# Kernel optimization log

Hardware: AMD Instinct MI355X
Metric: run time of the kernel (lower is better)

The kernel has to match this reference:

```python
import jax, jax.numpy as jnp
import numpy as np

B, S, D = 2, 2048, 1024
H, DK = 16, 64          # heads, d_k (= d_v)
DH = 4096               # FFN hidden
EPS = 1e-5


def _layer_norm(x, gamma, beta):
    mu = jnp.mean(x, axis=-1, keepdims=True)
    var = jnp.var(x, axis=-1, keepdims=True)
    return (x - mu) * jax.lax.rsqrt(var + EPS) * gamma + beta


def setup_inputs() -> dict:
    key = jax.random.key(0)
    ks = jax.random.split(key, 8)
    s = lambda fan_in: 1.0 / np.sqrt(fan_in)
    return {
        "x": jax.random.normal(ks[0], (B, S, D), dtype=jnp.float32),
        # NOTE: source module uses W_q for queries, keys AND values (bug kept faithfully),
        # so W_k / W_v are never used and are not materialized.
        "Wq": jax.random.normal(ks[1], (D, H * DK), dtype=jnp.float32) * s(D),
        "bq": jnp.zeros((H * DK,), dtype=jnp.float32),
        "Wo": jax.random.normal(ks[2], (H * DK, D), dtype=jnp.float32) * s(H * DK),
        "bo": jnp.zeros((D,), dtype=jnp.float32),
        "ln1_g": jnp.ones((D,), dtype=jnp.float32),
        "ln1_b": jnp.zeros((D,), dtype=jnp.float32),
        "W1": jax.random.normal(ks[3], (D, DH), dtype=jnp.float32) * s(D),
        "b1": jnp.zeros((DH,), dtype=jnp.float32),
        "W2": jax.random.normal(ks[4], (DH, D), dtype=jnp.float32) * s(DH),
        "b2": jnp.zeros((D,), dtype=jnp.float32),
        "ln2_g": jnp.ones((D,), dtype=jnp.float32),
        "ln2_b": jnp.zeros((D,), dtype=jnp.float32),
    }


def reference(x, Wq, bq, Wo, bo, ln1_g, ln1_b, W1, b1, W2, b2, ln2_g, ln2_b):
    residual = x
    # projections: q, k, v all use W_q (faithful to source)
    q = (x @ Wq + bq).reshape(B, S, H, DK)
    k = (x @ Wq + bq).reshape(B, S, H, DK)
    v = (x @ Wq + bq).reshape(B, S, H, DK)
    # scores scaled by sqrt(sequence_length), as in the source
    scale = 1.0 / jnp.sqrt(jnp.float32(S))
    scores = jnp.einsum("bqhd,bkhd->bhqk", q, k) * scale
    probs = jax.nn.softmax(scores, axis=-1)
    attn = jnp.einsum("bhqk,bkhd->bqhd", probs, v).reshape(B, S, H * DK)
    attn = attn @ Wo + bo
    # dropout is identity in eval mode
    x = _layer_norm(attn + residual, ln1_g, ln1_b)
    residual = x
    h = jax.nn.relu(x @ W1 + b1)
    x = h @ W2 + b2
    x = _layer_norm(x + residual, ln2_g, ln2_b)
    return x
```

## Files before the change

kernel.cpp:

```cpp
#include <hip/hip_runtime.h>
#include <stdint.h>


typedef unsigned short u16;
typedef __attribute__((ext_vector_type(8))) short v8s;
typedef __attribute__((ext_vector_type(4))) float v4f;

#define AS1 __attribute__((address_space(1)))
#define AS3 __attribute__((address_space(3)))

__device__ __forceinline__ void gl_lds16(const u16* g, u16* l) {
  __builtin_amdgcn_global_load_lds((const AS1 void*)g, (AS3 void*)l, 16, 0, 0);
}

__device__ __forceinline__ float bf2f(u16 u) {
  union { uint32_t i; float f; } v; v.i = ((uint32_t)u) << 16; return v.f;
}
__device__ __forceinline__ u16 f2bf(float f) {
  union { float f; uint32_t i; } v; v.f = f;
  uint32_t x = v.i;
  return (u16)((x + 0x7FFFu + ((x >> 16) & 1u)) >> 16);
}
__device__ __forceinline__ uint32_t fbits(float f) {
  union { float f; uint32_t u; } v; v.f = f; return v.u;
}

__global__ __launch_bounds__(256) void cvt_f2b(
    const float* __restrict__ src, u16* __restrict__ dst, int n4) {
  int i = (blockIdx.x * 256 + threadIdx.x);
  if (i < n4) {
    float4 v = *(const float4*)(src + (size_t)i * 4);
    ushort4 o;
    o.x = f2bf(v.x); o.y = f2bf(v.y); o.z = f2bf(v.z); o.w = f2bf(v.w);
    *(ushort4*)(dst + (size_t)i * 4) = o;
  }
}

__global__ __launch_bounds__(256) void transpose_f2b(
    const float* __restrict__ src, u16* __restrict__ dst,
    int R, int C, int ld_s, int ld_d) {
  __shared__ float tile[32][33];
  const int tx = threadIdx.x & 31, ty = threadIdx.x >> 5;
  const int c0 = blockIdx.x * 32, r0 = blockIdx.y * 32;
#pragma unroll
  for (int j = 0; j < 32; j += 8)
    tile[ty + j][tx] = src[(size_t)(r0 + ty + j) * ld_s + c0 + tx];
  __syncthreads();
#pragma unroll
  for (int j = 0; j < 32; j += 8)
    dst[(size_t)(c0 + ty + j) * ld_d + r0 + tx] = f2bf(tile[tx][ty + j]);
}

__global__ __launch_bounds__(256) void transpose_b2b(
    const u16* __restrict__ src, u16* __restrict__ dst,
    int R, int C, int ld_s, int ld_d) {
  __shared__ u16 tile[32][33];
  const int tx = threadIdx.x & 31, ty = threadIdx.x >> 5;
  const int c0 = blockIdx.x * 32, r0 = blockIdx.y * 32;
#pragma unroll
  for (int j = 0; j < 32; j += 8)
    tile[ty + j][tx] = src[(size_t)(r0 + ty + j) * ld_s + c0 + tx];
  __syncthreads();
#pragma unroll
  for (int j = 0; j < 32; j += 8)
    dst[(size_t)(c0 + ty + j) * ld_d + r0 + tx] = tile[tx][ty + j];
}

__global__ __launch_bounds__(256) void gemm_g1(
    const u16* __restrict__ A, const u16* __restrict__ Bt,
    const float* __restrict__ bias, void* __restrict__ C,
    int M, int N, int K, int relu, int accum, int out_f32) {
  __shared__ u16 As[2][4096];
  __shared__ u16 Bs[2][4096];
  const int tid = threadIdx.x;
  const int w = tid >> 6, l = tid & 63;
  const int lane16 = l & 15, kgrp = l >> 4;
  const int m0 = blockIdx.y * 128, n0 = blockIdx.x * 128;
  const int wr = (w >> 1) * 64, wc = (w & 1) * 64;

  const int sr = w * 32 + (l >> 2);
  const int sc = l & 3;
  const int sgc = sc ^ ((sr & 3) ^ ((sr >> 2) & 3));
  const u16* gA = A + (size_t)(m0 + sr) * K + 8 * sgc;
  const u16* gB = Bt + (size_t)(n0 + sr) * K + 8 * sgc;
  const size_t rstep = (size_t)16 * K;
  const int fl = (lane16 & 3) ^ ((lane16 >> 2) & 3);

  v4f acc[4][4];
#pragma unroll
  for (int i = 0; i < 4; i++)
#pragma unroll
    for (int j = 0; j < 4; j++)
#pragma unroll
      for (int r = 0; r < 4; r++) acc[i][j][r] = 0.f;

  gl_lds16(gA, &As[0][w * 1024]);
  gl_lds16(gA + rstep, &As[0][w * 1024 + 512]);
  gl_lds16(gB, &Bs[0][w * 1024]);
  gl_lds16(gB + rstep, &Bs[0][w * 1024 + 512]);

  int cur = 0;
  for (int k0 = 0; k0 < K; k0 += 32) {
    __syncthreads();
    if (k0 + 32 < K) {
      int nxt = cur ^ 1;
      gl_lds16(gA + k0 + 32, &As[nxt][w * 1024]);
      gl_lds16(gA + k0 + 32 + rstep, &As[nxt][w * 1024 + 512]);
      gl_lds16(gB + k0 + 32, &Bs[nxt][w * 1024]);
      gl_lds16(gB + k0 + 32 + rstep, &Bs[nxt][w * 1024 + 512]);
    }
    v8s a[4], b[4];
#pragma unroll
    for (int mi = 0; mi < 4; mi++)
      a[mi] = *(const v8s*)(&As[cur][(wr + mi * 16 + lane16) * 32 + 8 * (kgrp ^ fl)]);
#pragma unroll
    for (int ni = 0; ni < 4; ni++)
      b[ni] = *(const v8s*)(&Bs[cur][(wc + ni * 16 + lane16) * 32 + 8 * (kgrp ^ fl)]);
#pragma unroll
    for (int mi = 0; mi < 4; mi++)
#pragma unroll
      for (int ni = 0; ni < 4; ni++)
        acc[mi][ni] = __builtin_amdgcn_mfma_f32_16x16x32_bf16(a[mi], b[ni], acc[mi][ni], 0, 0, 0);
    cur ^= 1;
  }

#pragma unroll
  for (int ni = 0; ni < 4; ni++) {
    int col = n0 + wc + ni * 16 + lane16;
    float bv = bias ? bias[col] : 0.f;
#pragma unroll
    for (int mi = 0; mi < 4; mi++) {
      int row = m0 + wr + mi * 16 + kgrp * 4;
#pragma unroll
      for (int r = 0; r < 4; r++) {
        float v = acc[mi][ni][r] + bv;
        if (relu) v = fmaxf(v, 0.f);
        size_t idx = (size_t)(row + r) * N + col;
        if (out_f32) {
          float* Cf = (float*)C;
          if (accum) v += Cf[idx];
          Cf[idx] = v;
        } else {
          ((u16*)C)[idx] = f2bf(v);
        }
      }
    }
  }
}

__global__ __launch_bounds__(256) void gemm_g2(
    const u16* __restrict__ A, const u16* __restrict__ Bt,
    const float* __restrict__ bias, void* __restrict__ C,
    int M, int N, int K, int relu, int accum, int out_f32) {
  __shared__ u16 As[2][4096];
  __shared__ u16 Bs[2][2048];
  const int tid = threadIdx.x;
  const int w = tid >> 6, l = tid & 63;
  const int lane16 = l & 15, kgrp = l >> 4;
  const int m0 = blockIdx.y * 128, n0 = blockIdx.x * 64;
  const int wr = (w >> 1) * 64, wc = (w & 1) * 32;

  const int srA = w * 32 + (l >> 2);
  const int srB = w * 16 + (l >> 2);
  const int sc = l & 3;
  const int gcA = sc ^ ((srA & 3) ^ ((srA >> 2) & 3));
  const int gcB = sc ^ ((srB & 3) ^ ((srB >> 2) & 3));
  const u16* gA = A + (size_t)(m0 + srA) * K + 8 * gcA;
  const u16* gB = Bt + (size_t)(n0 + srB) * K + 8 * gcB;
  const size_t rstep = (size_t)16 * K;
  const int fl = (lane16 & 3) ^ ((lane16 >> 2) & 3);

  v4f acc[4][2];
#pragma unroll
  for (int i = 0; i < 4; i++)
#pragma unroll
    for (int j = 0; j < 2; j++)
#pragma unroll
      for (int r = 0; r < 4; r++) acc[i][j][r] = 0.f;

  gl_lds16(gA, &As[0][w * 1024]);
  gl_lds16(gA + rstep, &As[0][w * 1024 + 512]);
  gl_lds16(gB, &Bs[0][w * 512]);

  int cur = 0;
  for (int k0 = 0; k0 < K; k0 += 32) {
    __syncthreads();
    if (k0 + 32 < K) {
      int nxt = cur ^ 1;
      gl_lds16(gA + k0 + 32, &As[nxt][w * 1024]);
      gl_lds16(gA + k0 + 32 + rstep, &As[nxt][w * 1024 + 512]);
      gl_lds16(gB + k0 + 32, &Bs[nxt][w * 512]);
    }
    v8s a[4], b[2];
#pragma unroll
    for (int mi = 0; mi < 4; mi++)
      a[mi] = *(const v8s*)(&As[cur][(wr + mi * 16 + lane16) * 32 + 8 * (kgrp ^ fl)]);
#pragma unroll
    for (int ni = 0; ni < 2; ni++)
      b[ni] = *(const v8s*)(&Bs[cur][(wc + ni * 16 + lane16) * 32 + 8 * (kgrp ^ fl)]);
#pragma unroll
    for (int mi = 0; mi < 4; mi++)
#pragma unroll
      for (int ni = 0; ni < 2; ni++)
        acc[mi][ni] = __builtin_amdgcn_mfma_f32_16x16x32_bf16(a[mi], b[ni], acc[mi][ni], 0, 0, 0);
    cur ^= 1;
  }

#pragma unroll
  for (int ni = 0; ni < 2; ni++) {
    int col = n0 + wc + ni * 16 + lane16;
    float bv = bias ? bias[col] : 0.f;
#pragma unroll
    for (int mi = 0; mi < 4; mi++) {
      int row = m0 + wr + mi * 16 + kgrp * 4;
#pragma unroll
      for (int r = 0; r < 4; r++) {
        float v = acc[mi][ni][r] + bv;
        if (relu) v = fmaxf(v, 0.f);
        size_t idx = (size_t)(row + r) * N + col;
        if (out_f32) {
          float* Cf = (float*)C;
          if (accum) v += Cf[idx];
          Cf[idx] = v;
        } else {
          ((u16*)C)[idx] = f2bf(v);
        }
      }
    }
  }
}

__global__ __launch_bounds__(256) void attn_kernel(
    const u16* __restrict__ Q,
    const u16* __restrict__ Qt,
    u16* __restrict__ O) {
  __shared__ u16 KV[2][8192];
  __shared__ __align__(16) u16 Ps[4][2304];
  const int tid = threadIdx.x;
  const int w = tid >> 6, l = tid & 63;
  const int l16 = l & 15, kgrp = l >> 4;
  const int bh = blockIdx.y, b = bh >> 4, h = bh & 15;
  const int q0 = blockIdx.x * 128;
  const size_t rowQ = (size_t)(b * 2048 + q0 + w * 32);
  const float cexp = 1.4426950408889634f / 45.254833995939045f;

  const int srow = w * 8 + (l >> 3);
  const int sch8 = 8 * ((l & 7) ^ (srow & 7));
  const u16* gK0 = Q + (size_t)(b * 2048 + srow) * 1024 + h * 64 + sch8;
  const u16* gK1 = gK0 + (size_t)32 * 1024;
  const u16* gV0 = Qt + (size_t)(h * 64 + srow) * 4096 + b * 2048 + sch8;
  const u16* gV1 = gV0 + (size_t)32 * 4096;

  v8s qb[2][2];
#pragma unroll
  for (int nj = 0; nj < 2; nj++)
#pragma unroll
    for (int ks = 0; ks < 2; ks++) {
      v8s t = *(const v8s*)(Q + (rowQ + nj * 16 + l16) * 1024 + h * 64 + ks * 32 + kgrp * 8);
#pragma unroll
      for (int j = 0; j < 8; j++) t[j] = (short)f2bf(bf2f((u16)t[j]) * cexp);
      qb[nj][ks] = t;
    }

  v4f o[2][4];
  float ls[2] = {0.f, 0.f};
#pragma unroll
  for (int i = 0; i < 2; i++)
#pragma unroll
    for (int j = 0; j < 4; j++)
#pragma unroll
      for (int r = 0; r < 4; r++) o[i][j][r] = 0.f;

  gl_lds16(gK0, &KV[0][w * 512]);
  gl_lds16(gK1, &KV[0][2048 + w * 512]);
  gl_lds16(gV0, &KV[0][4096 + w * 512]);
  gl_lds16(gV1, &KV[0][4096 + 2048 + w * 512]);

  u16* Pw = &Ps[w][0];
  int cur = 0;
  for (int kb = 0; kb < 2048; kb += 64) {
    __syncthreads();
    if (kb + 64 < 2048) {
      int nxt = cur ^ 1;
      gl_lds16(gK0 + (size_t)(kb + 64) * 1024, &KV[nxt][w * 512]);
      gl_lds16(gK1 + (size_t)(kb + 64) * 1024, &KV[nxt][2048 + w * 512]);
      gl_lds16(gV0 + (kb + 64), &KV[nxt][4096 + w * 512]);
      gl_lds16(gV1 + (kb + 64), &KV[nxt][4096 + 2048 + w * 512]);
    }
    const u16* Ks = &KV[cur][0];
    const u16* Vt = &KV[cur][4096];

    v4f st[4][2];
#pragma unroll
    for (int i = 0; i < 4; i++)
#pragma unroll
      for (int j = 0; j < 2; j++)
#pragma unroll
        for (int r = 0; r < 4; r++) st[i][j][r] = 0.f;
#pragma unroll
    for (int ks = 0; ks < 2; ks++) {
      v8s ka[4];
#pragma unroll
      for (int mi = 0; mi < 4; mi++)
        ka[mi] = *(const v8s*)(Ks + (mi * 16 + l16) * 64 + 8 * ((ks * 4 + kgrp) ^ (l16 & 7)));
#pragma unroll
      for (int mi = 0; mi < 4; mi++)
#pragma unroll
        for (int nj = 0; nj < 2; nj++)
          st[mi][nj] = __builtin_amdgcn_mfma_f32_16x16x32_bf16(ka[mi], qb[nj][ks], st[mi][nj], 0, 0, 0);
    }

#pragma unroll
    for (int mi = 0; mi < 4; mi++)
#pragma unroll
      for (int nj = 0; nj < 2; nj++) {
        float p0 = __builtin_amdgcn_exp2f(st[mi][nj][0]);
        float p1 = __builtin_amdgcn_exp2f(st[mi][nj][1]);
        float p2 = __builtin_amdgcn_exp2f(st[mi][nj][2]);
        float p3 = __builtin_amdgcn_exp2f(st[mi][nj][3]);
        ls[nj] += (p0 + p1) + (p2 + p3);
        uint2 pk;
        pk.x = __builtin_amdgcn_perm(fbits(p1), fbits(p0), 0x07060302u);
        pk.y = __builtin_amdgcn_perm(fbits(p3), fbits(p2), 0x07060302u);
        *(uint2*)(Pw + (nj * 16 + l16) * 72 + mi * 16 + kgrp * 4) = pk;
      }

#pragma unroll
    for (int t = 0; t < 2; t++) {
      v8s pa[2], vb[4];
#pragma unroll
      for (int nj = 0; nj < 2; nj++)
        pa[nj] = *(const v8s*)(Pw + (nj * 16 + l16) * 72 + t * 32 + kgrp * 8);
#pragma unroll
      for (int ni = 0; ni < 4; ni++)
        vb[ni] = *(const v8s*)(Vt + (ni * 16 + l16) * 64 + 8 * ((t * 4 + kgrp) ^ (l16 & 7)));
#pragma unroll
      for (int nj = 0; nj < 2; nj++)
#pragma unroll
        for (int ni = 0; ni < 4; ni++)
          o[nj][ni] = __builtin_amdgcn_mfma_f32_16x16x32_bf16(pa[nj], vb[ni], o[nj][ni], 0, 0, 0);
    }
    cur ^= 1;
  }

#pragma unroll
  for (int nj = 0; nj < 2; nj++) {
    float t = ls[nj];
    t += __shfl_xor(t, 16, 64);
    t += __shfl_xor(t, 32, 64);
    ls[nj] = t;
  }

#pragma unroll
  for (int nj = 0; nj < 2; nj++) {
#pragma unroll
    for (int r = 0; r < 4; r++) {
      float den = __shfl(ls[nj], kgrp * 4 + r, 64);
      float rden = 1.f / den;
#pragma unroll
      for (int ni = 0; ni < 4; ni++) {
        O[(rowQ + nj * 16 + kgrp * 4 + r) * 1024 + h * 64 + ni * 16 + l16] =
            f2bf(o[nj][ni][r] * rden);
      }
    }
  }
}

__global__ __launch_bounds__(256) void ln_residual(
    const void* __restrict__ Y, const void* __restrict__ Xr,
    const float* __restrict__ g, const float* __restrict__ bb,
    void* __restrict__ out, int yf, int xf, int of) {
  const int row = blockIdx.x, tid = threadIdx.x;
  const size_t base = (size_t)row * 1024;
  float v[4], s = 0.f, sq = 0.f;
#pragma unroll
  for (int i = 0; i < 4; i++) {
    int c = tid + i * 256;
    float ya = yf ? ((const float*)Y)[base + c] : bf2f(((const u16*)Y)[base + c]);
    float xa = xf ? ((const float*)Xr)[base + c] : bf2f(((const u16*)Xr)[base + c]);
    float x = ya + xa;
    v[i] = x; s += x; sq += x * x;
  }
#pragma unroll
  for (int off = 32; off >= 1; off >>= 1) {
    s += __shfl_down(s, off, 64);
    sq += __shfl_down(sq, off, 64);
  }
  __shared__ float rs[4], rq[4];
  const int w = tid >> 6, l = tid & 63;
  if (l == 0) { rs[w] = s; rq[w] = sq; }
  __syncthreads();
  s = rs[0] + rs[1] + rs[2] + rs[3];
  sq = rq[0] + rq[1] + rq[2] + rq[3];
  const float mu = s * (1.f / 1024.f);
  const float var = sq * (1.f / 1024.f) - mu * mu;
  const float rstd = rsqrtf(var + 1e-5f);
#pragma unroll
  for (int i = 0; i < 4; i++) {
    int c = tid + i * 256;
    float r = (v[i] - mu) * rstd * g[c] + bb[c];
    if (of) ((float*)out)[base + c] = r;
    else ((u16*)out)[base + c] = f2bf(r);
  }
}

extern "C" void kernel_launch(void* const* d_in, const int* in_sizes, int n_in,
                              void* d_out, int out_size, void* d_ws, size_t ws_size,
                              hipStream_t stream) {
  const float* x   = (const float*)d_in[0];
  const float* Wq  = (const float*)d_in[1];
  const float* bq  = (const float*)d_in[2];
  const float* Wo  = (const float*)d_in[3];
  const float* bo  = (const float*)d_in[4];
  const float* g1  = (const float*)d_in[5];
  const float* be1 = (const float*)d_in[6];
  const float* W1  = (const float*)d_in[7];
  const float* b1  = (const float*)d_in[8];
  const float* W2  = (const float*)d_in[9];
  const float* b2  = (const float*)d_in[10];
  const float* g2  = (const float*)d_in[11];
  const float* be2 = (const float*)d_in[12];
  float* out = (float*)d_out;
  u16* ws  = (u16*)d_ws;

  const size_t M1 = 1048576;
  dim3 blk(256);
  const bool big = ws_size >= (size_t)37 * M1 * 2;

  if (big) {
    u16* xb   = ws + 0;
    u16* Qb   = ws + 4 * M1;
    u16* Qt   = ws + 8 * M1;
    u16* WqT  = ws + 12 * M1;
    u16* W1T  = ws + 13 * M1;
    u16* W2T  = ws + 17 * M1;
    u16* Hh   = ws + 21 * M1;
    u16* attn = xb;  u16* Yb = Qt;  u16* x1 = Qb;  u16* WoT = WqT;

    cvt_f2b<<<dim3(4096), blk, 0, stream>>>(x, xb, 1048576);
    transpose_f2b<<<dim3(32, 32), blk, 0, stream>>>(Wq, WqT, 1024, 1024, 1024, 1024);
    gemm_g2<<<dim3(16, 32), blk, 0, stream>>>(xb, WqT, bq, Qb, 4096, 1024, 1024, 0, 0, 0);

    transpose_b2b<<<dim3(32, 128), blk, 0, stream>>>(Qb, Qt, 4096, 1024, 1024, 4096);
    attn_kernel<<<dim3(16, 32), blk, 0, stream>>>(Qb, Qt, attn);

    transpose_f2b<<<dim3(32, 32), blk, 0, stream>>>(Wo, WoT, 1024, 1024, 1024, 1024);
    gemm_g2<<<dim3(16, 32), blk, 0, stream>>>(attn, WoT, bo, Yb, 4096, 1024, 1024, 0, 0, 0);
    ln_residual<<<dim3(4096), blk, 0, stream>>>(Yb, x, g1, be1, x1, 0, 1, 0);

    transpose_f2b<<<dim3(128, 32), blk, 0, stream>>>(W1, W1T, 1024, 4096, 4096, 1024);
    gemm_g1<<<dim3(32, 32), blk, 0, stream>>>(x1, W1T, b1, Hh, 4096, 4096, 1024, 1, 0, 0);
    transpose_f2b<<<dim3(32, 128), blk, 0, stream>>>(W2, W2T, 4096, 1024, 1024, 4096);
    gemm_g2<<<dim3(16, 32), blk, 0, stream>>>(Hh, W2T, b2, out, 4096, 1024, 4096, 0, 0, 1);

    ln_residual<<<dim3(4096), blk, 0, stream>>>(out, x1, g2, be2, out, 1, 0, 1);
  } else {
    u16* xb   = ws + 0;
    u16* Qb   = ws + 4 * M1;
    u16* Qt   = ws + 8 * M1;
    u16* attn = xb;  u16* Yb = Qt;  u16* x1 = Qb;  u16* Hc = xb;
    u16* Wt1  = ws + 12 * M1;
    u16* Wt2  = ws + 13 * M1;

    cvt_f2b<<<dim3(4096), blk, 0, stream>>>(x, xb, 1048576);
    transpose_f2b<<<dim3(32, 32), blk, 0, stream>>>(Wq, Wt1, 1024, 1024, 1024, 1024);
    gemm_g2<<<dim3(16, 32), blk, 0, stream>>>(xb, Wt1, bq, Qb, 4096, 1024, 1024, 0, 0, 0);

    transpose_b2b<<<dim3(32, 128), blk, 0, stream>>>(Qb, Qt, 4096, 1024, 1024, 4096);
    attn_kernel<<<dim3(16, 32), blk, 0, stream>>>(Qb, Qt, attn);

    transpose_f2b<<<dim3(32, 32), blk, 0, stream>>>(Wo, Wt2, 1024, 1024, 1024, 1024);
    gemm_g2<<<dim3(16, 32), blk, 0, stream>>>(attn, Wt2, bo, Yb, 4096, 1024, 1024, 0, 0, 0);
    ln_residual<<<dim3(4096), blk, 0, stream>>>(Yb, x, g1, be1, x1, 0, 1, 0);

    for (int c = 0; c < 4; c++) {
      transpose_f2b<<<dim3(32, 32), blk, 0, stream>>>(W1 + (size_t)c * 1024, Wt1,
                                                      1024, 1024, 4096, 1024);
      gemm_g2<<<dim3(16, 32), blk, 0, stream>>>(x1, Wt1, b1 + (size_t)c * 1024, Hc,
                                                4096, 1024, 1024, 1, 0, 0);
      transpose_f2b<<<dim3(32, 32), blk, 0, stream>>>(W2 + (size_t)c * M1, Wt2,
                                                      1024, 1024, 1024, 1024);
      gemm_g2<<<dim3(16, 32), blk, 0, stream>>>(Hc, Wt2, (c == 0) ? b2 : (const float*)nullptr,
                                                out, 4096, 1024, 1024, 0, (c > 0) ? 1 : 0, 1);
    }
    ln_residual<<<dim3(4096), blk, 0, stream>>>(out, x1, g2, be2, out, 1, 0, 1);
  }
}
```

Baseline: 374.5 us.

## Split-K the FFN down-projection with atomics and widen gemm_g2 K-tile to 64

The W2 GEMM (K=4096) now runs on the 128x128 gemm_g1 kernel with a 4-way split over K. Each split accumulates fp32 results into the output with atomicAdd, and only split 0 adds the bias; the output is zeroed with a memset first. This raises block count and tile reuse for the long-K GEMM. gemm_g2 is also rewritten to stage 64-wide K tiles with an 8-way XOR swizzle, which halves the barriers per K. The cost is atomic traffic, an extra memset, and nondeterministic summation order.

```diff
diff --git a/kernel.cpp b/kernel.cpp
--- a/kernel.cpp
+++ b/kernel.cpp
@@ -69,21 +69,23 @@
 __global__ __launch_bounds__(256) void gemm_g1(
     const u16* __restrict__ A, const u16* __restrict__ Bt,
     const float* __restrict__ bias, void* __restrict__ C,
-    int M, int N, int K, int relu, int accum, int out_f32) {
+    int M, int N, int ldk, int klen, int relu, int accum, int out_f32,
+    int atomic) {
   __shared__ u16 As[2][4096];
   __shared__ u16 Bs[2][4096];
   const int tid = threadIdx.x;
   const int w = tid >> 6, l = tid & 63;
   const int lane16 = l & 15, kgrp = l >> 4;
   const int m0 = blockIdx.y * 128, n0 = blockIdx.x * 128;
+  const int k_begin = blockIdx.z * klen;
   const int wr = (w >> 1) * 64, wc = (w & 1) * 64;
 
   const int sr = w * 32 + (l >> 2);
   const int sc = l & 3;
   const int sgc = sc ^ ((sr & 3) ^ ((sr >> 2) & 3));
-  const u16* gA = A + (size_t)(m0 + sr) * K + 8 * sgc;
-  const u16* gB = Bt + (size_t)(n0 + sr) * K + 8 * sgc;
-  const size_t rstep = (size_t)16 * K;
+  const u16* gA = A + (size_t)(m0 + sr) * ldk + k_begin + 8 * sgc;
+  const u16* gB = Bt + (size_t)(n0 + sr) * ldk + k_begin + 8 * sgc;
+  const size_t rstep = (size_t)16 * ldk;
   const int fl = (lane16 & 3) ^ ((lane16 >> 2) & 3);
 
   v4f acc[4][4];
@@ -100,9 +102,9 @@
   gl_lds16(gB + rstep, &Bs[0][w * 1024 + 512]);
 
   int cur = 0;
-  for (int k0 = 0; k0 < K; k0 += 32) {
+  for (int k0 = 0; k0 < klen; k0 += 32) {
     __syncthreads();
-    if (k0 + 32 < K) {
+    if (k0 + 32 < klen) {
       int nxt = cur ^ 1;
       gl_lds16(gA + k0 + 32, &As[nxt][w * 1024]);
       gl_lds16(gA + k0 + 32 + rstep, &As[nxt][w * 1024 + 512]);
@@ -127,6 +129,104 @@
 #pragma unroll
   for (int ni = 0; ni < 4; ni++) {
     int col = n0 + wc + ni * 16 + lane16;
+    float bv = (bias && k_begin == 0) ? bias[col] : 0.f;
+#pragma unroll
+    for (int mi = 0; mi < 4; mi++) {
+      int row = m0 + wr + mi * 16 + kgrp * 4;
+#pragma unroll
+      for (int r = 0; r < 4; r++) {
+        float v = acc[mi][ni][r] + bv;
+        if (relu) v = fmaxf(v, 0.f);
+        size_t idx = (size_t)(row + r) * N + col;
+        if (atomic) {
+          atomicAdd(&((float*)C)[idx], v);
+        } else if (out_f32) {
+          float* Cf = (float*)C;
+          if (accum) v += Cf[idx];
+          Cf[idx] = v;
+        } else {
+          ((u16*)C)[idx] = f2bf(v);
+        }
+      }
+    }
+  }
+}
+
+__global__ __launch_bounds__(256) void gemm_g2(
+    const u16* __restrict__ A, const u16* __restrict__ Bt,
+    const float* __restrict__ bias, void* __restrict__ C,
+    int M, int N, int K, int relu, int accum, int out_f32) {
+  __shared__ u16 As[2][8192];
+  __shared__ u16 Bs[2][4096];
+  const int tid = threadIdx.x;
+  const int w = tid >> 6, l = tid & 63;
+  const int l16 = l & 15, kgrp = l >> 4;
+  const int m0 = blockIdx.y * 128, n0 = blockIdx.x * 64;
+  const int wr = (w >> 1) * 64, wc = (w & 1) * 32;
+
+  const int srow = w * 8 + (l >> 3);
+  const u16* gA[4];
+#pragma unroll
+  for (int i = 0; i < 4; i++) {
+    int r = i * 32 + srow;
+    gA[i] = A + (size_t)(m0 + r) * K + 8 * ((l & 7) ^ (r & 7));
+  }
+  const u16* gB[2];
+#pragma unroll
+  for (int i = 0; i < 2; i++) {
+    int r = i * 32 + srow;
+    gB[i] = Bt + (size_t)(n0 + r) * K + 8 * ((l & 7) ^ (r & 7));
+  }
+
+  v4f acc[4][2];
+#pragma unroll
+  for (int i = 0; i < 4; i++)
+#pragma unroll
+    for (int j = 0; j < 2; j++)
+#pragma unroll
+      for (int r = 0; r < 4; r++) acc[i][j][r] = 0.f;
+
+#pragma unroll
+  for (int i = 0; i < 4; i++) gl_lds16(gA[i], &As[0][(i * 256 + w * 64) * 8]);
+#pragma unroll
+  for (int i = 0; i < 2; i++) gl_lds16(gB[i], &Bs[0][(i * 256 + w * 64) * 8]);
+
+  int cur = 0;
+  for (int k0 = 0; k0 < K; k0 += 64) {
+    __syncthreads();
+    if (k0 + 64 < K) {
+      int nxt = cur ^ 1;
+#pragma unroll
+      for (int i = 0; i < 4; i++)
+        gl_lds16(gA[i] + k0 + 64, &As[nxt][(i * 256 + w * 64) * 8]);
+#pragma unroll
+      for (int i = 0; i < 2; i++)
+        gl_lds16(gB[i] + k0 + 64, &Bs[nxt][(i * 256 + w * 64) * 8]);
+    }
+    v8s a[4][2], b[2][2];
+#pragma unroll
+    for (int ks = 0; ks < 2; ks++) {
+      int ch = 8 * ((ks * 4 + kgrp) ^ (l16 & 7));
+#pragma unroll
+      for (int mi = 0; mi < 4; mi++)
+        a[mi][ks] = *(const v8s*)(&As[cur][(wr + mi * 16 + l16) * 64 + ch]);
+#pragma unroll
+      for (int ni = 0; ni < 2; ni++)
+        b[ni][ks] = *(const v8s*)(&Bs[cur][(wc + ni * 16 + l16) * 64 + ch]);
+    }
+#pragma unroll
+    for (int ks = 0; ks < 2; ks++)
+#pragma unroll
+      for (int mi = 0; mi < 4; mi++)
+#pragma unroll
+        for (int ni = 0; ni < 2; ni++)
+          acc[mi][ni] = __builtin_amdgcn_mfma_f32_16x16x32_bf16(a[mi][ks], b[ni][ks], acc[mi][ni], 0, 0, 0);
+    cur ^= 1;
+  }
+
+#pragma unroll
+  for (int ni = 0; ni < 2; ni++) {
+    int col = n0 + wc + ni * 16 + l16;
     float bv = bias ? bias[col] : 0.f;
 #pragma unroll
     for (int mi = 0; mi < 4; mi++) {
@@ -148,91 +248,8 @@
   }
 }
 
-__global__ __launch_bounds__(256) void gemm_g2(
-    const u16* __restrict__ A, const u16* __restrict__ Bt,
-    const float* __restrict__ bias, void* __restrict__ C,
-    int M, int N, int K, int relu, int accum, int out_f32) {
-  __shared__ u16 As[2][4096];
-  __shared__ u16 Bs[2][2048];
-  const int tid = threadIdx.x;
-  const int w = tid >> 6, l = tid & 63;
-  const int lane16 = l & 15, kgrp = l >> 4;
-  const int m0 = blockIdx.y * 128, n0 = blockIdx.x * 64;
-  const int wr = (w >> 1) * 64, wc = (w & 1) * 32;
-
-  const int srA = w * 32 + (l >> 2);
-  const int srB = w * 16 + (l >> 2);
-  const int sc = l & 3;
-  const int gcA = sc ^ ((srA & 3) ^ ((srA >> 2) & 3));
-  const int gcB = sc ^ ((srB & 3) ^ ((srB >> 2) & 3));
-  const u16* gA = A + (size_t)(m0 + srA) * K + 8 * gcA;
-  const u16* gB = Bt + (size_t)(n0 + srB) * K + 8 * gcB;
-  const size_t rstep = (size_t)16 * K;
-  const int fl = (lane16 & 3) ^ ((lane16 >> 2) & 3);
-
-  v4f acc[4][2];
-#pragma unroll
-  for (int i = 0; i < 4; i++)
-#pragma unroll
-    for (int j = 0; j < 2; j++)
-#pragma unroll
-      for (int r = 0; r < 4; r++) acc[i][j][r] = 0.f;
-
-  gl_lds16(gA, &As[0][w * 1024]);
-  gl_lds16(gA + rstep, &As[0][w * 1024 + 512]);
-  gl_lds16(gB, &Bs[0][w * 512]);
-
-  int cur = 0;
-  for (int k0 = 0; k0 < K; k0 += 32) {
-    __syncthreads();
-    if (k0 + 32 < K) {
-      int nxt = cur ^ 1;
-      gl_lds16(gA + k0 + 32, &As[nxt][w * 1024]);
-      gl_lds16(gA + k0 + 32 + rstep, &As[nxt][w * 1024 + 512]);
-      gl_lds16(gB + k0 + 32, &Bs[nxt][w * 512]);
-    }
-    v8s a[4], b[2];
-#pragma unroll
-    for (int mi = 0; mi < 4; mi++)
-      a[mi] = *(const v8s*)(&As[cur][(wr + mi * 16 + lane16) * 32 + 8 * (kgrp ^ fl)]);
-#pragma unroll
-    for (int ni = 0; ni < 2; ni++)
-      b[ni] = *(const v8s*)(&Bs[cur][(wc + ni * 16 + lane16) * 32 + 8 * (kgrp ^ fl)]);
-#pragma unroll
-    for (int mi = 0; mi < 4; mi++)
-#pragma unroll
-      for (int ni = 0; ni < 2; ni++)
-        acc[mi][ni] = __builtin_amdgcn_mfma_f32_16x16x32_bf16(a[mi], b[ni], acc[mi][ni], 0, 0, 0);
-    cur ^= 1;
-  }
-
-#pragma unroll
-  for (int ni = 0; ni < 2; ni++) {
-    int col = n0 + wc + ni * 16 + lane16;
-    float bv = bias ? bias[col] : 0.f;
-#pragma unroll
-    for (int mi = 0; mi < 4; mi++) {
-      int row = m0 + wr + mi * 16 + kgrp * 4;
-#pragma unroll
-      for (int r = 0; r < 4; r++) {
-        float v = acc[mi][ni][r] + bv;
-        if (relu) v = fmaxf(v, 0.f);
-        size_t idx = (size_t)(row + r) * N + col;
-        if (out_f32) {
-          float* Cf = (float*)C;
-          if (accum) v += Cf[idx];
-          Cf[idx] = v;
-        } else {
-          ((u16*)C)[idx] = f2bf(v);
-        }
-      }
-    }
-  }
-}
-
 __global__ __launch_bounds__(256) void attn_kernel(
-    const u16* __restrict__ Q,
-    const u16* __restrict__ Qt,
+    const u16* __restrict__ Q, const u16* __restrict__ Qt,
     u16* __restrict__ O) {
   __shared__ u16 KV[2][8192];
   __shared__ __align__(16) u16 Ps[4][2304];
@@ -437,6 +454,8 @@
     u16* Hh   = ws + 21 * M1;
     u16* attn = xb;  u16* Yb = Qt;  u16* x1 = Qb;  u16* WoT = WqT;
 
+    hipMemsetAsync(out, 0, (size_t)out_size * sizeof(float), stream);
+
     cvt_f2b<<<dim3(4096), blk, 0, stream>>>(x, xb, 1048576);
     transpose_f2b<<<dim3(32, 32), blk, 0, stream>>>(Wq, WqT, 1024, 1024, 1024, 1024);
     gemm_g2<<<dim3(16, 32), blk, 0, stream>>>(xb, WqT, bq, Qb, 4096, 1024, 1024, 0, 0, 0);
@@ -449,9 +468,11 @@
     ln_residual<<<dim3(4096), blk, 0, stream>>>(Yb, x, g1, be1, x1, 0, 1, 0);
 
     transpose_f2b<<<dim3(128, 32), blk, 0, stream>>>(W1, W1T, 1024, 4096, 4096, 1024);
-    gemm_g1<<<dim3(32, 32), blk, 0, stream>>>(x1, W1T, b1, Hh, 4096, 4096, 1024, 1, 0, 0);
+    gemm_g1<<<dim3(32, 32, 1), blk, 0, stream>>>(x1, W1T, b1, Hh, 4096, 4096,
+                                                 1024, 1024, 1, 0, 0, 0);
     transpose_f2b<<<dim3(32, 128), blk, 0, stream>>>(W2, W2T, 4096, 1024, 1024, 4096);
-    gemm_g2<<<dim3(16, 32), blk, 0, stream>>>(Hh, W2T, b2, out, 4096, 1024, 4096, 0, 0, 1);
+    gemm_g1<<<dim3(8, 32, 4), blk, 0, stream>>>(Hh, W2T, b2, out, 4096, 1024,
+                                                4096, 1024, 0, 0, 1, 1);
 
     ln_residual<<<dim3(4096), blk, 0, stream>>>(out, x1, g2, be2, out, 1, 0, 1);
   } else {
```

Result: slower. 391.4 us (+4.5%).
